# Performance work log

Hardware: AMD Instinct MI355X
Metric: run time of the kernel (lower is better)

Reference implementation:

```python
import jax, jax.numpy as jnp
import numpy as np

N_HEAD = 16
N_STATE = 1024
D_HEAD = N_STATE // N_HEAD
B, T = 4, 2048


def setup_inputs() -> dict:
    key = jax.random.key(0)
    ks = jax.random.split(key, 9)
    x = jax.random.normal(ks[0], (B, T, N_STATE), dtype=jnp.float32)
    # causal additive mask, (T, T)
    neg = jnp.float32(-1e9)
    mask = jnp.where(jnp.tril(jnp.ones((T, T), dtype=bool)), 0.0, neg).astype(jnp.float32)
    s = 0.02  # keep activations in a sane range (module uses torch.randn init)
    Wq = jax.random.normal(ks[1], (N_STATE, N_STATE), dtype=jnp.float32) * s
    bq = jax.random.normal(ks[2], (N_STATE,), dtype=jnp.float32) * s
    Wk = jax.random.normal(ks[3], (N_STATE, N_STATE), dtype=jnp.float32) * s
    Wv = jax.random.normal(ks[4], (N_STATE, N_STATE), dtype=jnp.float32) * s
    bv = jax.random.normal(ks[5], (N_STATE,), dtype=jnp.float32) * s
    Wo = jax.random.normal(ks[6], (N_STATE, N_STATE), dtype=jnp.float32) * s
    bo = jax.random.normal(ks[7], (N_STATE,), dtype=jnp.float32) * s
    return {"x": x, "mask": mask, "Wq": Wq, "bq": bq, "Wk": Wk,
            "Wv": Wv, "bv": bv, "Wo": Wo, "bo": bo}


def reference(x, mask, Wq, bq, Wk, Wv, bv, Wo, bo):
    n, t, _ = x.shape
    scale = D_HEAD ** -0.25
    # projections: Linear stores weight as (out, in), applies x @ W.T
    q = x @ Wq.T + bq
    k = x @ Wk.T          # key has no bias
    v = x @ Wv.T + bv
    # (N, H, T, d)
    q = q.reshape(n, t, N_HEAD, D_HEAD).transpose(0, 2, 1, 3) * scale
    k = k.reshape(n, t, N_HEAD, D_HEAD).transpose(0, 2, 1, 3) * scale
    v = v.reshape(n, t, N_HEAD, D_HEAD).transpose(0, 2, 1, 3)
    qk = jnp.einsum('bhqd,bhkd->bhqk', q, k)
    qk = qk + mask[:t, :t]
    attn = jax.nn.softmax(qk, axis=-1)
    qkv = jnp.einsum('bhqk,bhkd->bhqd', attn, v)
    qkv = qkv.transpose(0, 2, 1, 3).reshape(n, t, N_STATE)
    return qkv @ Wo.T + bo
```

## Files before the change

### kernel.cpp

```cpp
#include <hip/hip_runtime.h>
#include <stdint.h>

#define DEVI __device__ __forceinline__

typedef float        f32x4   __attribute__((ext_vector_type(4)));
typedef float        f32x16  __attribute__((ext_vector_type(16)));
typedef __bf16       bf16x8  __attribute__((ext_vector_type(8)));
typedef unsigned short u16x8 __attribute__((ext_vector_type(8)));
typedef uint32_t     u32x2   __attribute__((ext_vector_type(2)));
typedef uint32_t     u32x4   __attribute__((ext_vector_type(4)));

static constexpr int TSEQ   = 2048;
static constexpr int NSTATE = 1024;
static constexpr int NHEAD  = 16;
static constexpr int DHEAD  = 64;
static constexpr int BATCH  = 4;
static constexpr int MROWS  = BATCH * TSEQ;
static constexpr float QSCALE = 0.125f * 1.44269504088896340736f;
static constexpr float DEFER_THR = 8.0f * 1.44269504088896340736f;

DEVI unsigned short f2bf(float f) {
  union { float f; uint32_t u; } v; v.f = f;
  return (unsigned short)((v.u + 0x7fffu + ((v.u >> 16) & 1u)) >> 16);
}

DEVI uint32_t cvt_pk_bf16(float lo, float hi) {
  uint32_t r;
  asm("v_cvt_pk_bf16_f32 %0, %1, %2" : "=v"(r) : "v"(lo), "v"(hi));
  return r;
}

DEVI f32x4 mfma16(u16x8 a, u16x8 b, f32x4 c) {
  return __builtin_amdgcn_mfma_f32_16x16x32_bf16(
      __builtin_bit_cast(bf16x8, a), __builtin_bit_cast(bf16x8, b), c, 0, 0, 0);
}
DEVI f32x16 mfma32(u16x8 a, u16x8 b, f32x16 c) {
  return __builtin_amdgcn_mfma_f32_32x32x16_bf16(
      __builtin_bit_cast(bf16x8, a), __builtin_bit_cast(bf16x8, b), c, 0, 0, 0);
}

__global__ void cvt_kernel(const float* __restrict__ in,
                           unsigned short* __restrict__ out, int n4) {
  int i = blockIdx.x * blockDim.x + threadIdx.x;
  const int stride = gridDim.x * blockDim.x;
  for (; i < n4; i += stride) {
    const float4 f = ((const float4*)in)[i];
    ushort4 o;
    o.x = f2bf(f.x); o.y = f2bf(f.y); o.z = f2bf(f.z); o.w = f2bf(f.w);
    ((ushort4*)out)[i] = o;
  }
}

__global__ void cvt4_kernel(const float* __restrict__ w0, const float* __restrict__ w1,
                            const float* __restrict__ w2, const float* __restrict__ w3,
                            unsigned short* __restrict__ o0, unsigned short* __restrict__ o1,
                            unsigned short* __restrict__ o2, unsigned short* __restrict__ o3) {
  const int per = NSTATE * NSTATE / 4;
  int i = blockIdx.x * blockDim.x + threadIdx.x;
  const int stride = gridDim.x * blockDim.x;
  for (; i < 4 * per; i += stride) {
    const int wi = i / per, j = i - wi * per;
    const float* src = (wi == 0) ? w0 : (wi == 1) ? w1 : (wi == 2) ? w2 : w3;
    unsigned short* dst = (wi == 0) ? o0 : (wi == 1) ? o1 : (wi == 2) ? o2 : o3;
    const float4 f = ((const float4*)src)[j];
    ushort4 o;
    o.x = f2bf(f.x); o.y = f2bf(f.y); o.z = f2bf(f.z); o.w = f2bf(f.w);
    ((ushort4*)dst)[j] = o;
  }
}

__global__ __launch_bounds__(512)
void gemm_qkv256(const unsigned short* __restrict__ A,
                 const unsigned short* __restrict__ Wqkv,
                 const float* __restrict__ bq, const float* __restrict__ bv,
                 unsigned short* __restrict__ Oqkv)
{
  __shared__ __align__(16) unsigned short As[2][256 * 64];
  __shared__ __align__(16) unsigned short Bs[2][256 * 64];
  const int t = threadIdx.x;
  const int lane = t & 63, wid = t >> 6;
  const int fr = lane & 15, fq = lane >> 4;
  const int wi  = blockIdx.x >> 2;
  const int n0w = (blockIdx.x & 3) * 256;
  const int m0  = blockIdx.y * 256;
  const int wm = wid >> 2, wn = wid & 3;
  const unsigned short* Bw = Wqkv + ((size_t)wi << 20);
  unsigned short* Cq = Oqkv + ((size_t)wi << 23);

  f32x4 acc[8][4] = {};

  const int srow = t >> 3, sg = t & 7;
  const unsigned short* ag = A  + (size_t)(m0  + srow) * NSTATE + sg * 8;
  const unsigned short* bg = Bw + (size_t)(n0w + srow) * NSTATE + sg * 8;
  int wof[4];
  #pragma unroll
  for (int s = 0; s < 4; ++s) {
    const int r = srow + s * 64;
    wof[s] = r * 64 + ((sg ^ (r & 7)) * 8);
  }

  u16x8 sa[4], sb[4];
  #pragma unroll
  for (int s = 0; s < 4; ++s) {
    sa[s] = *(const u16x8*)(ag + (size_t)s * 64 * NSTATE);
    sb[s] = *(const u16x8*)(bg + (size_t)s * 64 * NSTATE);
  }
  #pragma unroll
  for (int s = 0; s < 4; ++s) {
    *(u16x8*)(&As[0][wof[s]]) = sa[s];
    *(u16x8*)(&Bs[0][wof[s]]) = sb[s];
  }

  for (int kt = 0; kt < NSTATE / 64; ++kt) {
    const int cur = kt & 1;
    __syncthreads();
    const bool pre = (kt + 1) < NSTATE / 64;
    if (pre) {
      const int ko = (kt + 1) * 64;
      #pragma unroll
      for (int s = 0; s < 4; ++s) {
        sa[s] = *(const u16x8*)(ag + ko + (size_t)s * 64 * NSTATE);
        sb[s] = *(const u16x8*)(bg + ko + (size_t)s * 64 * NSTATE);
      }
    }
    #pragma unroll
    for (int kk = 0; kk < 2; ++kk) {
      u16x8 af[8], bf[4];
      #pragma unroll
      for (int i = 0; i < 8; ++i) {
        const int r = wm * 128 + i * 16 + fr;
        const int g = (kk * 4 + fq) ^ (r & 7);
        af[i] = *(const u16x8*)(&As[cur][r * 64 + g * 8]);
      }
      #pragma unroll
      for (int j = 0; j < 4; ++j) {
        const int r = wn * 64 + j * 16 + fr;
        const int g = (kk * 4 + fq) ^ (r & 7);
        bf[j] = *(const u16x8*)(&Bs[cur][r * 64 + g * 8]);
      }
      __builtin_amdgcn_s_setprio(1);
      #pragma unroll
      for (int i = 0; i < 8; ++i)
        #pragma unroll
        for (int j = 0; j < 4; ++j)
          acc[i][j] = mfma16(af[i], bf[j], acc[i][j]);
      __builtin_amdgcn_s_setprio(0);
    }
    if (pre) {
      #pragma unroll
      for (int s = 0; s < 4; ++s) {
        *(u16x8*)(&As[cur ^ 1][wof[s]]) = sa[s];
        *(u16x8*)(&Bs[cur ^ 1][wof[s]]) = sb[s];
      }
    }
  }

  const int h = (n0w + wn * 64) >> 6;
  #pragma unroll
  for (int j = 0; j < 4; ++j) {
    const int d = j * 16 + fr;
    const int ncol = n0w + wn * 64 + d;
    const float bj = (wi == 1) ? 0.0f : ((wi == 0) ? bq[ncol] : bv[ncol]);
    #pragma unroll
    for (int i = 0; i < 8; ++i) {
      #pragma unroll
      for (int r = 0; r < 4; ++r) {
        const int row = m0 + wm * 128 + i * 16 + fq * 4 + r;
        const int bb = row >> 11, tt = row & (TSEQ - 1);
        float v = acc[i][j][r] + bj;
        if (wi == 0) v *= QSCALE;
        Cq[(((size_t)(bb * NHEAD + h)) * TSEQ + tt) * DHEAD + d] = f2bf(v);
      }
    }
  }
}

__global__ __launch_bounds__(512)
void gemm_out256(const unsigned short* __restrict__ A,
                 const unsigned short* __restrict__ Bw,
                 const float* __restrict__ bias,
                 float* __restrict__ Co)
{
  __shared__ __align__(16) unsigned short As[2][128 * 64];
  __shared__ __align__(16) unsigned short Bs[2][256 * 64];
  const int t = threadIdx.x;
  const int lane = t & 63, wid = t >> 6;
  const int fr = lane & 15, fq = lane >> 4;
  const int n0 = blockIdx.x * 256;
  const int m0 = blockIdx.y * 128;
  const int wm = wid >> 2, wn = wid & 3;

  f32x4 acc[4][4] = {};

  const int srow = t >> 3, sg = t & 7;
  const unsigned short* ag = A  + (size_t)(m0 + srow) * NSTATE + sg * 8;
  const unsigned short* bg = Bw + (size_t)(n0 + srow) * NSTATE + sg * 8;
  int wof[4];
  #pragma unroll
  for (int s = 0; s < 4; ++s) {
    const int r = srow + s * 64;
    wof[s] = r * 64 + ((sg ^ (r & 7)) * 8);
  }

  u16x8 sa[2], sb[4];
  #pragma unroll
  for (int s = 0; s < 2; ++s)
    sa[s] = *(const u16x8*)(ag + (size_t)s * 64 * NSTATE);
  #pragma unroll
  for (int s = 0; s < 4; ++s)
    sb[s] = *(const u16x8*)(bg + (size_t)s * 64 * NSTATE);
  #pragma unroll
  for (int s = 0; s < 2; ++s) *(u16x8*)(&As[0][wof[s]]) = sa[s];
  #pragma unroll
  for (int s = 0; s < 4; ++s) *(u16x8*)(&Bs[0][wof[s]]) = sb[s];

  for (int kt = 0; kt < NSTATE / 64; ++kt) {
    const int cur = kt & 1;
    __syncthreads();
    const bool pre = (kt + 1) < NSTATE / 64;
    if (pre) {
      const int ko = (kt + 1) * 64;
      #pragma unroll
      for (int s = 0; s < 2; ++s)
        sa[s] = *(const u16x8*)(ag + ko + (size_t)s * 64 * NSTATE);
      #pragma unroll
      for (int s = 0; s < 4; ++s)
        sb[s] = *(const u16x8*)(bg + ko + (size_t)s * 64 * NSTATE);
    }
    #pragma unroll
    for (int kk = 0; kk < 2; ++kk) {
      u16x8 af[4], bf[4];
      #pragma unroll
      for (int i = 0; i < 4; ++i) {
        const int r = wm * 64 + i * 16 + fr;
        const int g = (kk * 4 + fq) ^ (r & 7);
        af[i] = *(const u16x8*)(&As[cur][r * 64 + g * 8]);
      }
      #pragma unroll
      for (int j = 0; j < 4; ++j) {
        const int r = wn * 64 + j * 16 + fr;
        const int g = (kk * 4 + fq) ^ (r & 7);
        bf[j] = *(const u16x8*)(&Bs[cur][r * 64 + g * 8]);
      }
      __builtin_amdgcn_s_setprio(1);
      #pragma unroll
      for (int i = 0; i < 4; ++i)
        #pragma unroll
        for (int j = 0; j < 4; ++j)
          acc[i][j] = mfma16(af[i], bf[j], acc[i][j]);
      __builtin_amdgcn_s_setprio(0);
    }
    if (pre) {
      #pragma unroll
      for (int s = 0; s < 2; ++s) *(u16x8*)(&As[cur ^ 1][wof[s]]) = sa[s];
      #pragma unroll
      for (int s = 0; s < 4; ++s) *(u16x8*)(&Bs[cur ^ 1][wof[s]]) = sb[s];
    }
  }

  #pragma unroll
  for (int j = 0; j < 4; ++j) {
    const int col = n0 + wn * 64 + j * 16 + fr;
    const float bj = bias[col];
    #pragma unroll
    for (int i = 0; i < 4; ++i) {
      const int row0 = m0 + wm * 64 + i * 16 + fq * 4;
      #pragma unroll
      for (int r = 0; r < 4; ++r)
        Co[(size_t)(row0 + r) * NSTATE + col] = acc[i][j][r] + bj;
    }
  }
}

__global__ __launch_bounds__(256)
void flash_attn(const unsigned short* __restrict__ Qg,
                const unsigned short* __restrict__ Kg,
                const unsigned short* __restrict__ Vg,
                unsigned short* __restrict__ O)
{
  const int bh = blockIdx.x;
  const int b  = bh >> 4, h = bh & 15;
  const int t  = threadIdx.x, lane = t & 63, w = t >> 6;
  const int lq = lane & 31, hi = lane >> 5;
  const size_t hoff = (size_t)bh * TSEQ * DHEAD;
  const unsigned short* Qp = Qg + hoff;
  const unsigned short* Kp = Kg + hoff;
  const unsigned short* Vp = Vg + hoff;

  __shared__ __align__(16) unsigned short Kb[2][64 * 64];
  __shared__ __align__(16) unsigned short Vb[2][64 * 64];

  const int skr = t >> 2, skg = t & 3;
  const int svk2 = (t & 31) * 2;
  const int svd  = (t >> 5) * 8;

  #define STAGE_V(buf, va, vb)                                              \
    do {                                                                    \
      const u32x4 vau = __builtin_bit_cast(u32x4, va);                      \
      const u32x4 vbu = __builtin_bit_cast(u32x4, vb);                      \
      _Pragma("unroll")                                                     \
      for (int j = 0; j < 4; ++j) {                                         \
        const uint32_t pe = __builtin_amdgcn_perm(vbu[j], vau[j], 0x05040100); \
        const uint32_t po = __builtin_amdgcn_perm(vbu[j], vau[j], 0x07060302); \
        *(uint32_t*)(&Vb[buf][(svd + 2 * j) * 64 + (svk2 ^ ((2 * j) << 3))]) = pe; \
        *(uint32_t*)(&Vb[buf][(svd + 2 * j + 1) * 64 + (svk2 ^ ((2 * j + 1) << 3))]) = po; \
      }                                                                     \
    } while (0)

  for (int pass = 0; pass < 2; ++pass) {
    const int qb = pass ? (int)blockIdx.y : 15 - (int)blockIdx.y;
    const int qw   = qb * 128 + w * 32;
    const int qrow = qw + lq;

    u16x8 qf[4];
    #pragma unroll
    for (int c = 0; c < 4; ++c)
      qf[c] = *(const u16x8*)(Qp + (size_t)qrow * DHEAD + c * 16 + hi * 8);

    f32x16 oacc[2] = {};
    float m_r = -1e30f, l_r = 0.0f;

    const int nt = (qb + 1) * 2;

    {
      const u16x8 kr0 = *(const u16x8*)(Kp + (size_t)skr * DHEAD + skg * 16);
      const u16x8 kr1 = *(const u16x8*)(Kp + (size_t)skr * DHEAD + skg * 16 + 8);
      const u16x8 va  = *(const u16x8*)(Vp + (size_t)svk2 * DHEAD + svd);
      const u16x8 vb  = *(const u16x8*)(Vp + (size_t)(svk2 + 1) * DHEAD + svd);
      *(u16x8*)(&Kb[0][skr * 64 + (((skg * 2)     ^ (skr & 7)) << 3)]) = kr0;
      *(u16x8*)(&Kb[0][skr * 64 + (((skg * 2 + 1) ^ (skr & 7)) << 3)]) = kr1;
      STAGE_V(0, va, vb);
    }
    __syncthreads();

    for (int kt = 0; kt < nt; ++kt) {
      const int k0 = kt * 64, cur = kt & 1;
      const bool pre = (kt + 1 < nt);
      u16x8 krn0, krn1, van, vbn;
      if (pre) {
        const int k0n = k0 + 64;
        krn0 = *(const u16x8*)(Kp + (size_t)(k0n + skr) * DHEAD + skg * 16);
        krn1 = *(const u16x8*)(Kp + (size_t)(k0n + skr) * DHEAD + skg * 16 + 8);
        van  = *(const u16x8*)(Vp + (size_t)(k0n + svk2) * DHEAD + svd);
        vbn  = *(const u16x8*)(Vp + (size_t)(k0n + svk2 + 1) * DHEAD + svd);
      }

      if (k0 < qw + 32) {
        f32x16 s[2];
        __builtin_amdgcn_s_setprio(1);
        #pragma unroll
        for (int t32 = 0; t32 < 2; ++t32) {
          if (k0 + t32 * 32 < qw + 32) {
            f32x16 z = {};
            #pragma unroll
            for (int c = 0; c < 4; ++c) {
              const u16x8 kf = *(const u16x8*)(
                  &Kb[cur][(t32 * 32 + lq) * 64 + (((2 * c + hi) ^ (lane & 7)) << 3)]);
              z = mfma32(kf, qf[c], z);
            }
            s[t32] = z;
          } else {
            #pragma unroll
            for (int r = 0; r < 16; ++r) s[t32][r] = -1e30f;
          }
        }
        __builtin_amdgcn_s_setprio(0);
        if (k0 + 63 > qw) {
          #pragma unroll
          for (int t32 = 0; t32 < 2; ++t32)
            #pragma unroll
            for (int r = 0; r < 16; ++r) {
              const int kk = k0 + t32 * 32 + (r & 3) + 8 * (r >> 2) + 4 * hi;
              if (kk > qrow) s[t32][r] = -1e30f;
            }
        }

        float mx = fmaxf(s[0][14], s[0][15]);
        #pragma unroll
        for (int r = 0; r < 14; r += 2) mx = fmaxf(fmaxf(mx, s[0][r]), s[0][r + 1]);
        #pragma unroll
        for (int r = 0; r < 16; r += 2) mx = fmaxf(fmaxf(mx, s[1][r]), s[1][r + 1]);
        mx = fmaxf(mx, __shfl_xor(mx, 32));

        if (__any(mx > m_r + DEFER_THR)) {
          const float mnew = fmaxf(m_r, mx);
          const float corr = exp2f(m_r - mnew);
          #pragma unroll
          for (int ds = 0; ds < 2; ++ds)
            #pragma unroll
            for (int r = 0; r < 16; ++r) oacc[ds][r] *= corr;
          l_r *= corr;
          m_r = mnew;
        }

        float ps = 0.0f;
        uint32_t pk[2][8];
        #pragma unroll
        for (int t32 = 0; t32 < 2; ++t32)
          #pragma unroll
          for (int m2 = 0; m2 < 8; ++m2) {
            const float pa = exp2f(s[t32][2 * m2]     - m_r);
            const float pb = exp2f(s[t32][2 * m2 + 1] - m_r);
            ps += pa + pb;
            pk[t32][m2] = cvt_pk_bf16(pa, pb);
          }
        ps += __shfl_xor(ps, 32);
        l_r += ps;

        uint32_t pf[2][2][4];
        #pragma unroll
        for (int t32 = 0; t32 < 2; ++t32)
          #pragma unroll
          for (int hf = 0; hf < 2; ++hf) {
            const u32x2 r02 = __builtin_amdgcn_permlane32_swap(
                pk[t32][hf * 4 + 0], pk[t32][hf * 4 + 2], false, false);
            const u32x2 r13 = __builtin_amdgcn_permlane32_swap(
                pk[t32][hf * 4 + 1], pk[t32][hf * 4 + 3], false, false);
            pf[t32][hf][0] = r02.x; pf[t32][hf][2] = r02.y;
            pf[t32][hf][1] = r13.x; pf[t32][hf][3] = r13.y;
          }

        __builtin_amdgcn_s_setprio(1);
        #pragma unroll
        for (int c = 0; c < 4; ++c) {
          if (k0 + 16 * c < qw + 32) {
            const u32x4 pw = {pf[c >> 1][c & 1][0], pf[c >> 1][c & 1][1],
                              pf[c >> 1][c & 1][2], pf[c >> 1][c & 1][3]};
            const u16x8 pv = __builtin_bit_cast(u16x8, pw);
            #pragma unroll
            for (int ds = 0; ds < 2; ++ds) {
              const u16x8 vf = *(const u16x8*)(
                  &Vb[cur][(ds * 32 + lq) * 64 + (((2 * c + hi) ^ (lq & 7)) << 3)]);
              oacc[ds] = mfma32(vf, pv, oacc[ds]);
            }
          }
        }
        __builtin_amdgcn_s_setprio(0);
      }

      if (pre) {
        *(u16x8*)(&Kb[cur ^ 1][skr * 64 + (((skg * 2)     ^ (skr & 7)) << 3)]) = krn0;
        *(u16x8*)(&Kb[cur ^ 1][skr * 64 + (((skg * 2 + 1) ^ (skr & 7)) << 3)]) = krn1;
        STAGE_V(cur ^ 1, van, vbn);
      }
      __syncthreads();
    }

    const float inv = 1.0f / l_r;
    const size_t base = ((size_t)(b * TSEQ + qrow)) * NSTATE + h * DHEAD;
    #pragma unroll
    for (int ds = 0; ds < 2; ++ds)
      #pragma unroll
      for (int m2 = 0; m2 < 8; ++m2) {
        const int d = ds * 32 + 2 * (m2 & 1) + 8 * (m2 >> 1) + 4 * hi;
        *(uint32_t*)(O + base + d) =
            cvt_pk_bf16(oacc[ds][2 * m2] * inv, oacc[ds][2 * m2 + 1] * inv);
      }
  }
  #undef STAGE_V
}

extern "C" void kernel_launch(void* const* d_in, const int* in_sizes, int n_in,
                              void* d_out, int out_size, void* d_ws, size_t ws_size,
                              hipStream_t stream)
{
  (void)in_sizes; (void)n_in; (void)out_size; (void)ws_size;
  const float* x  = (const float*)d_in[0];
  const float* Wq = (const float*)d_in[2];
  const float* bq = (const float*)d_in[3];
  const float* Wk = (const float*)d_in[4];
  const float* Wv = (const float*)d_in[5];
  const float* bv = (const float*)d_in[6];
  const float* Wo = (const float*)d_in[7];
  const float* bo = (const float*)d_in[8];

  char* ws = (char*)d_ws;
  unsigned short* xb  = (unsigned short*)(ws);
  unsigned short* wqb = (unsigned short*)(ws + (16u << 20));
  unsigned short* wkb = wqb + (1u << 20);
  unsigned short* wvb = wkb + (1u << 20);
  unsigned short* wob = wvb + (1u << 20);
  unsigned short* qb_ = (unsigned short*)(ws + (24u << 20));
  unsigned short* kb_ = (unsigned short*)(ws + (40u << 20));
  unsigned short* vb_ = (unsigned short*)(ws + (56u << 20));

  cvt_kernel<<<2048, 256, 0, stream>>>(x,  xb,  MROWS * NSTATE / 4);
  cvt4_kernel<<<2048, 256, 0, stream>>>(Wq, Wk, Wv, Wo, wqb, wkb, wvb, wob);

  gemm_qkv256<<<dim3(12, MROWS / 256), 512, 0, stream>>>(xb, wqb, bq, bv, qb_);

  flash_attn<<<dim3(BATCH * NHEAD, 8), 256, 0, stream>>>(qb_, kb_, vb_, xb);

  gemm_out256<<<dim3(NSTATE / 256, MROWS / 128), 512, 0, stream>>>(xb, wob, bo, (float*)d_out);
}
```

Baseline: 202.6 us.

## Process both causal query blocks in one KV sweep and merge conversion kernels

The flash attention kernel now holds two query blocks (a long one and a short one) in registers at once and sweeps the K/V tiles a single time, applying each block's tile computation while the tiles are resident. Before, the two blocks ran in two separate passes that each reloaded K/V. This removes the duplicated K/V loads and staging, at the cost of doubling the accumulator and Q-fragment register footprint, which may lower occupancy. It also merges the x and weight bf16 conversion kernels into one launch and swaps exp2f for a raw v_exp_f32 instruction. An unused global-to-LDS load helper is added.

```diff
diff --git a/kernel.cpp b/kernel.cpp
--- a/kernel.cpp
+++ b/kernel.cpp
@@ -29,6 +29,11 @@
   asm("v_cvt_pk_bf16_f32 %0, %1, %2" : "=v"(r) : "v"(lo), "v"(hi));
   return r;
 }
+DEVI float fexp2(float x) {
+  float r;
+  asm("v_exp_f32 %0, %1" : "=v"(r) : "v"(x));
+  return r;
+}
 
 DEVI f32x4 mfma16(u16x8 a, u16x8 b, f32x4 c) {
   return __builtin_amdgcn_mfma_f32_16x16x32_bf16(
@@ -39,29 +44,34 @@
       __builtin_bit_cast(bf16x8, a), __builtin_bit_cast(bf16x8, b), c, 0, 0, 0);
 }
 
-__global__ void cvt_kernel(const float* __restrict__ in,
-                           unsigned short* __restrict__ out, int n4) {
+DEVI void gload_lds16(const void* g, void* l) {
+  __builtin_amdgcn_global_load_lds(
+      (const __attribute__((address_space(1))) void*)g,
+      (__attribute__((address_space(3))) void*)l, 16, 0, 0);
+}
+
+__global__ void cvt_all(const float* __restrict__ x,
+                        const float* __restrict__ w0, const float* __restrict__ w1,
+                        const float* __restrict__ w2, const float* __restrict__ w3,
+                        unsigned short* __restrict__ xb,
+                        unsigned short* __restrict__ wb)
+{
+  const int NX = (MROWS * NSTATE) / 4;
+  const int NW = (NSTATE * NSTATE) / 4;
+  const int total = NX + 4 * NW;
   int i = blockIdx.x * blockDim.x + threadIdx.x;
   const int stride = gridDim.x * blockDim.x;
-  for (; i < n4; i += stride) {
-    const float4 f = ((const float4*)in)[i];
-    ushort4 o;
-    o.x = f2bf(f.x); o.y = f2bf(f.y); o.z = f2bf(f.z); o.w = f2bf(f.w);
-    ((ushort4*)out)[i] = o;
-  }
-}
-
-__global__ void cvt4_kernel(const float* __restrict__ w0, const float* __restrict__ w1,
-                            const float* __restrict__ w2, const float* __restrict__ w3,
-                            unsigned short* __restrict__ o0, unsigned short* __restrict__ o1,
-                            unsigned short* __restrict__ o2, unsigned short* __restrict__ o3) {
-  const int per = NSTATE * NSTATE / 4;
-  int i = blockIdx.x * blockDim.x + threadIdx.x;
-  const int stride = gridDim.x * blockDim.x;
-  for (; i < 4 * per; i += stride) {
-    const int wi = i / per, j = i - wi * per;
-    const float* src = (wi == 0) ? w0 : (wi == 1) ? w1 : (wi == 2) ? w2 : w3;
-    unsigned short* dst = (wi == 0) ? o0 : (wi == 1) ? o1 : (wi == 2) ? o2 : o3;
+  for (; i < total; i += stride) {
+    const float* src;
+    unsigned short* dst;
+    int j;
+    if (i < NX) { src = x; dst = xb; j = i; }
+    else {
+      const int k = i - NX, wi = k >> 18;
+      src = (wi == 0) ? w0 : (wi == 1) ? w1 : (wi == 2) ? w2 : w3;
+      dst = wb + ((size_t)wi << 20);
+      j = k & (NW - 1);
+    }
     const float4 f = ((const float4*)src)[j];
     ushort4 o;
     o.x = f2bf(f.x); o.y = f2bf(f.y); o.z = f2bf(f.z); o.w = f2bf(f.w);
@@ -279,6 +289,8 @@
                 unsigned short* __restrict__ O)
 {
   const int bh = blockIdx.x;
+  const int y  = blockIdx.y;
+  const int qbA = 15 - y, qbB = y;
   const int b  = bh >> 4, h = bh & 15;
   const int t  = threadIdx.x, lane = t & 63, w = t >> 6;
   const int lq = lane & 31, hi = lane >> 5;
@@ -289,6 +301,19 @@
 
   __shared__ __align__(16) unsigned short Kb[2][64 * 64];
   __shared__ __align__(16) unsigned short Vb[2][64 * 64];
+
+  const int qwA = qbA * 128 + w * 32, qrowA = qwA + lq;
+  const int qwB = qbB * 128 + w * 32, qrowB = qwB + lq;
+
+  u16x8 qfA[4], qfB[4];
+  #pragma unroll
+  for (int c = 0; c < 4; ++c) {
+    qfA[c] = *(const u16x8*)(Qp + (size_t)qrowA * DHEAD + c * 16 + hi * 8);
+    qfB[c] = *(const u16x8*)(Qp + (size_t)qrowB * DHEAD + c * 16 + hi * 8);
+  }
+
+  f32x16 oaccA[2] = {}, oaccB[2] = {};
+  float mA = -1e30f, lA = 0.0f, mB = -1e30f, lB = 0.0f;
 
   const int skr = t >> 2, skg = t & 3;
   const int svk2 = (t & 31) * 2;
@@ -307,156 +332,155 @@
       }                                                                     \
     } while (0)
 
-  for (int pass = 0; pass < 2; ++pass) {
-    const int qb = pass ? (int)blockIdx.y : 15 - (int)blockIdx.y;
-    const int qw   = qb * 128 + w * 32;
-    const int qrow = qw + lq;
-
-    u16x8 qf[4];
-    #pragma unroll
-    for (int c = 0; c < 4; ++c)
-      qf[c] = *(const u16x8*)(Qp + (size_t)qrow * DHEAD + c * 16 + hi * 8);
-
-    f32x16 oacc[2] = {};
-    float m_r = -1e30f, l_r = 0.0f;
-
-    const int nt = (qb + 1) * 2;
-
-    {
-      const u16x8 kr0 = *(const u16x8*)(Kp + (size_t)skr * DHEAD + skg * 16);
-      const u16x8 kr1 = *(const u16x8*)(Kp + (size_t)skr * DHEAD + skg * 16 + 8);
-      const u16x8 va  = *(const u16x8*)(Vp + (size_t)svk2 * DHEAD + svd);
-      const u16x8 vb  = *(const u16x8*)(Vp + (size_t)(svk2 + 1) * DHEAD + svd);
-      *(u16x8*)(&Kb[0][skr * 64 + (((skg * 2)     ^ (skr & 7)) << 3)]) = kr0;
-      *(u16x8*)(&Kb[0][skr * 64 + (((skg * 2 + 1) ^ (skr & 7)) << 3)]) = kr1;
-      STAGE_V(0, va, vb);
+  #define ATTN_TILE(qw_, qrow_, qf_, oacc_, m_, l_)                          \
+    do {                                                                     \
+      f32x16 s[2];                                                           \
+      __builtin_amdgcn_s_setprio(1);                                         \
+      _Pragma("unroll")                                                      \
+      for (int t32 = 0; t32 < 2; ++t32) {                                    \
+        if (k0 + t32 * 32 < (qw_) + 32) {                                    \
+          f32x16 z = {};                                                     \
+          _Pragma("unroll")                                                  \
+          for (int c = 0; c < 4; ++c) {                                      \
+            const u16x8 kf = *(const u16x8*)(                                \
+                &Kb[cur][(t32 * 32 + lq) * 64 + (((2 * c + hi) ^ (lane & 7)) << 3)]); \
+            z = mfma32(kf, (qf_)[c], z);                                     \
+          }                                                                  \
+          s[t32] = z;                                                        \
+        } else {                                                             \
+          _Pragma("unroll")                                                  \
+          for (int r = 0; r < 16; ++r) s[t32][r] = -1e30f;                   \
+        }                                                                    \
+      }                                                                      \
+      __builtin_amdgcn_s_setprio(0);                                         \
+      if (k0 + 63 > (qw_)) {                                                 \
+        _Pragma("unroll")                                                    \
+        for (int t32 = 0; t32 < 2; ++t32)                                    \
+          _Pragma("unroll")                                                  \
+          for (int r = 0; r < 16; ++r) {                                     \
+            const int kk = k0 + t32 * 32 + (r & 3) + 8 * (r >> 2) + 4 * hi;  \
+            if (kk > (qrow_)) s[t32][r] = -1e30f;                            \
+          }                                                                  \
+      }                                                                      \
+      float mx = fmaxf(s[0][14], s[0][15]);                                  \
+      _Pragma("unroll")                                                      \
+      for (int r = 0; r < 14; r += 2) mx = fmaxf(fmaxf(mx, s[0][r]), s[0][r + 1]); \
+      _Pragma("unroll")                                                      \
+      for (int r = 0; r < 16; r += 2) mx = fmaxf(fmaxf(mx, s[1][r]), s[1][r + 1]); \
+      mx = fmaxf(mx, __shfl_xor(mx, 32));                                    \
+      if (__any(mx > (m_) + DEFER_THR)) {                                    \
+        const float mnew = fmaxf((m_), mx);                                  \
+        const float corr = fexp2((m_) - mnew);                               \
+        _Pragma("unroll")                                                    \
+        for (int ds = 0; ds < 2; ++ds)                                       \
+          _Pragma("unroll")                                                  \
+          for (int r = 0; r < 16; ++r) (oacc_)[ds][r] *= corr;               \
+        (l_) *= corr;                                                        \
+        (m_) = mnew;                                                         \
+      }                                                                      \
+      float ps = 0.0f;                                                       \
+      uint32_t pk[2][8];                                                     \
+      _Pragma("unroll")                                                      \
+      for (int t32 = 0; t32 < 2; ++t32)                                      \
+        _Pragma("unroll")                                                    \
+        for (int m2 = 0; m2 < 8; ++m2) {                                     \
+          const float pa = fexp2(s[t32][2 * m2]     - (m_));                 \
+          const float pb = fexp2(s[t32][2 * m2 + 1] - (m_));                 \
+          ps += pa + pb;                                                     \
+          pk[t32][m2] = cvt_pk_bf16(pa, pb);                                 \
+        }                                                                    \
+      ps += __shfl_xor(ps, 32);                                              \
+      (l_) += ps;                                                            \
+      uint32_t pf[2][2][4];                                                  \
+      _Pragma("unroll")                                                      \
+      for (int t32 = 0; t32 < 2; ++t32)                                      \
+        _Pragma("unroll")                                                    \
+        for (int hf = 0; hf < 2; ++hf) {                                     \
+          const u32x2 r02 = __builtin_amdgcn_permlane32_swap(                \
+              pk[t32][hf * 4 + 0], pk[t32][hf * 4 + 2], false, false);       \
+          const u32x2 r13 = __builtin_amdgcn_permlane32_swap(                \
+              pk[t32][hf * 4 + 1], pk[t32][hf * 4 + 3], false, false);       \
+          pf[t32][hf][0] = r02.x; pf[t32][hf][2] = r02.y;                    \
+          pf[t32][hf][1] = r13.x; pf[t32][hf][3] = r13.y;                    \
+        }                                                                    \
+      __builtin_amdgcn_s_setprio(1);                                         \
+      _Pragma("unroll")                                                      \
+      for (int c = 0; c < 4; ++c) {                                          \
+        if (k0 + 16 * c < (qw_) + 32) {                                      \
+          const u32x4 pw = {pf[c >> 1][c & 1][0], pf[c >> 1][c & 1][1],      \
+                            pf[c >> 1][c & 1][2], pf[c >> 1][c & 1][3]};     \
+          const u16x8 pv = __builtin_bit_cast(u16x8, pw);                    \
+          _Pragma("unroll")                                                  \
+          for (int ds = 0; ds < 2; ++ds) {                                   \
+            const u16x8 vf = *(const u16x8*)(                                \
+                &Vb[cur][(ds * 32 + lq) * 64 + (((2 * c + hi) ^ (lq & 7)) << 3)]); \
+            (oacc_)[ds] = mfma32(vf, pv, (oacc_)[ds]);                       \
+          }                                                                  \
+        }                                                                    \
+      }                                                                      \
+      __builtin_amdgcn_s_setprio(0);                                         \
+    } while (0)
+
+  {
+    const u16x8 kr0 = *(const u16x8*)(Kp + (size_t)skr * DHEAD + skg * 16);
+    const u16x8 kr1 = *(const u16x8*)(Kp + (size_t)skr * DHEAD + skg * 16 + 8);
+    const u16x8 va  = *(const u16x8*)(Vp + (size_t)svk2 * DHEAD + svd);
+    const u16x8 vb  = *(const u16x8*)(Vp + (size_t)(svk2 + 1) * DHEAD + svd);
+    *(u16x8*)(&Kb[0][skr * 64 + (((skg * 2)     ^ (skr & 7)) << 3)]) = kr0;
+    *(u16x8*)(&Kb[0][skr * 64 + (((skg * 2 + 1) ^ (skr & 7)) << 3)]) = kr1;
+    STAGE_V(0, va, vb);
+  }
+  __syncthreads();
+
+  const int nt = (qbA + 1) * 2;
+  for (int kt = 0; kt < nt; ++kt) {
+    const int k0 = kt * 64, cur = kt & 1;
+    const bool pre = (kt + 1 < nt);
+    u16x8 krn0, krn1, van, vbn;
+    if (pre) {
+      const int k0n = k0 + 64;
+      krn0 = *(const u16x8*)(Kp + (size_t)(k0n + skr) * DHEAD + skg * 16);
+      krn1 = *(const u16x8*)(Kp + (size_t)(k0n + skr) * DHEAD + skg * 16 + 8);
+      van  = *(const u16x8*)(Vp + (size_t)(k0n + svk2) * DHEAD + svd);
+      vbn  = *(const u16x8*)(Vp + (size_t)(k0n + svk2 + 1) * DHEAD + svd);
+    }
+
+    if (k0 < qwA + 32) ATTN_TILE(qwA, qrowA, qfA, oaccA, mA, lA);
+    if (k0 < qwB + 32) ATTN_TILE(qwB, qrowB, qfB, oaccB, mB, lB);
+
+    if (pre) {
+      *(u16x8*)(&Kb[cur ^ 1][skr * 64 + (((skg * 2)     ^ (skr & 7)) << 3)]) = krn0;
+      *(u16x8*)(&Kb[cur ^ 1][skr * 64 + (((skg * 2 + 1) ^ (skr & 7)) << 3)]) = krn1;
+      STAGE_V(cur ^ 1, van, vbn);
     }
     __syncthreads();
-
-    for (int kt = 0; kt < nt; ++kt) {
-      const int k0 = kt * 64, cur = kt & 1;
-      const bool pre = (kt + 1 < nt);
-      u16x8 krn0, krn1, van, vbn;
-      if (pre) {
-        const int k0n = k0 + 64;
-        krn0 = *(const u16x8*)(Kp + (size_t)(k0n + skr) * DHEAD + skg * 16);
-        krn1 = *(const u16x8*)(Kp + (size_t)(k0n + skr) * DHEAD + skg * 16 + 8);
-        van  = *(const u16x8*)(Vp + (size_t)(k0n + svk2) * DHEAD + svd);
-        vbn  = *(const u16x8*)(Vp + (size_t)(k0n + svk2 + 1) * DHEAD + svd);
-      }
-
-      if (k0 < qw + 32) {
-        f32x16 s[2];
-        __builtin_amdgcn_s_setprio(1);
-        #pragma unroll
-        for (int t32 = 0; t32 < 2; ++t32) {
-          if (k0 + t32 * 32 < qw + 32) {
-            f32x16 z = {};
-            #pragma unroll
-            for (int c = 0; c < 4; ++c) {
-              const u16x8 kf = *(const u16x8*)(
-                  &Kb[cur][(t32 * 32 + lq) * 64 + (((2 * c + hi) ^ (lane & 7)) << 3)]);
-              z = mfma32(kf, qf[c], z);
-            }
-            s[t32] = z;
-          } else {
-            #pragma unroll
-            for (int r = 0; r < 16; ++r) s[t32][r] = -1e30f;
-          }
-        }
-        __builtin_amdgcn_s_setprio(0);
-        if (k0 + 63 > qw) {
-          #pragma unroll
-          for (int t32 = 0; t32 < 2; ++t32)
-            #pragma unroll
-            for (int r = 0; r < 16; ++r) {
-              const int kk = k0 + t32 * 32 + (r & 3) + 8 * (r >> 2) + 4 * hi;
-              if (kk > qrow) s[t32][r] = -1e30f;
-            }
-        }
-
-        float mx = fmaxf(s[0][14], s[0][15]);
-        #pragma unroll
-        for (int r = 0; r < 14; r += 2) mx = fmaxf(fmaxf(mx, s[0][r]), s[0][r + 1]);
-        #pragma unroll
-        for (int r = 0; r < 16; r += 2) mx = fmaxf(fmaxf(mx, s[1][r]), s[1][r + 1]);
-        mx = fmaxf(mx, __shfl_xor(mx, 32));
-
-        if (__any(mx > m_r + DEFER_THR)) {
-          const float mnew = fmaxf(m_r, mx);
-          const float corr = exp2f(m_r - mnew);
-          #pragma unroll
-          for (int ds = 0; ds < 2; ++ds)
-            #pragma unroll
-            for (int r = 0; r < 16; ++r) oacc[ds][r] *= corr;
-          l_r *= corr;
-          m_r = mnew;
-        }
-
-        float ps = 0.0f;
-        uint32_t pk[2][8];
-        #pragma unroll
-        for (int t32 = 0; t32 < 2; ++t32)
-          #pragma unroll
-          for (int m2 = 0; m2 < 8; ++m2) {
-            const float pa = exp2f(s[t32][2 * m2]     - m_r);
-            const float pb = exp2f(s[t32][2 * m2 + 1] - m_r);
-            ps += pa + pb;
-            pk[t32][m2] = cvt_pk_bf16(pa, pb);
-          }
-        ps += __shfl_xor(ps, 32);
-        l_r += ps;
-
-        uint32_t pf[2][2][4];
-        #pragma unroll
-        for (int t32 = 0; t32 < 2; ++t32)
-          #pragma unroll
-          for (int hf = 0; hf < 2; ++hf) {
-            const u32x2 r02 = __builtin_amdgcn_permlane32_swap(
-                pk[t32][hf * 4 + 0], pk[t32][hf * 4 + 2], false, false);
-            const u32x2 r13 = __builtin_amdgcn_permlane32_swap(
-                pk[t32][hf * 4 + 1], pk[t32][hf * 4 + 3], false, false);
-            pf[t32][hf][0] = r02.x; pf[t32][hf][2] = r02.y;
-            pf[t32][hf][1] = r13.x; pf[t32][hf][3] = r13.y;
-          }
-
-        __builtin_amdgcn_s_setprio(1);
-        #pragma unroll
-        for (int c = 0; c < 4; ++c) {
-          if (k0 + 16 * c < qw + 32) {
-            const u32x4 pw = {pf[c >> 1][c & 1][0], pf[c >> 1][c & 1][1],
-                              pf[c >> 1][c & 1][2], pf[c >> 1][c & 1][3]};
-            const u16x8 pv = __builtin_bit_cast(u16x8, pw);
-            #pragma unroll
-            for (int ds = 0; ds < 2; ++ds) {
-              const u16x8 vf = *(const u16x8*)(
-                  &Vb[cur][(ds * 32 + lq) * 64 + (((2 * c + hi) ^ (lq & 7)) << 3)]);
-              oacc[ds] = mfma32(vf, pv, oacc[ds]);
-            }
-          }
-        }
-        __builtin_amdgcn_s_setprio(0);
-      }
-
-      if (pre) {
-        *(u16x8*)(&Kb[cur ^ 1][skr * 64 + (((skg * 2)     ^ (skr & 7)) << 3)]) = krn0;
-        *(u16x8*)(&Kb[cur ^ 1][skr * 64 + (((skg * 2 + 1) ^ (skr & 7)) << 3)]) = krn1;
-        STAGE_V(cur ^ 1, van, vbn);
-      }
-      __syncthreads();
-    }
-
-    const float inv = 1.0f / l_r;
-    const size_t base = ((size_t)(b * TSEQ + qrow)) * NSTATE + h * DHEAD;
+  }
+
+  {
+    const float inv = 1.0f / lA;
+    const size_t base = ((size_t)(b * TSEQ + qrowA)) * NSTATE + h * DHEAD;
     #pragma unroll
     for (int ds = 0; ds < 2; ++ds)
       #pragma unroll
       for (int m2 = 0; m2 < 8; ++m2) {
         const int d = ds * 32 + 2 * (m2 & 1) + 8 * (m2 >> 1) + 4 * hi;
         *(uint32_t*)(O + base + d) =
-            cvt_pk_bf16(oacc[ds][2 * m2] * inv, oacc[ds][2 * m2 + 1] * inv);
-      }
-  }
+            cvt_pk_bf16(oaccA[ds][2 * m2] * inv, oaccA[ds][2 * m2 + 1] * inv);
+      }
+  }
+  {
+    const float inv = 1.0f / lB;
+    const size_t base = ((size_t)(b * TSEQ + qrowB)) * NSTATE + h * DHEAD;
+    #pragma unroll
+    for (int ds = 0; ds < 2; ++ds)
+      #pragma unroll
+      for (int m2 = 0; m2 < 8; ++m2) {
+        const int d = ds * 32 + 2 * (m2 & 1) + 8 * (m2 >> 1) + 4 * hi;
+        *(uint32_t*)(O + base + d) =
+            cvt_pk_bf16(oaccB[ds][2 * m2] * inv, oaccB[ds][2 * m2 + 1] * inv);
+      }
+  }
+  #undef ATTN_TILE
   #undef STAGE_V
 }
 
@@ -477,15 +501,12 @@
   char* ws = (char*)d_ws;
   unsigned short* xb  = (unsigned short*)(ws);
   unsigned short* wqb = (unsigned short*)(ws + (16u << 20));
-  unsigned short* wkb = wqb + (1u << 20);
-  unsigned short* wvb = wkb + (1u << 20);
-  unsigned short* wob = wvb + (1u << 20);
+  unsigned short* wob = wqb + (3u << 20);
   unsigned short* qb_ = (unsigned short*)(ws + (24u << 20));
   unsigned short* kb_ = (unsigned short*)(ws + (40u << 20));
   unsigned short* vb_ = (unsigned short*)(ws + (56u << 20));
 
-  cvt_kernel<<<2048, 256, 0, stream>>>(x,  xb,  MROWS * NSTATE / 4);
-  cvt4_kernel<<<2048, 256, 0, stream>>>(Wq, Wk, Wv, Wo, wqb, wkb, wvb, wob);
+  cvt_all<<<2048, 256, 0, stream>>>(x, Wq, Wk, Wv, Wo, xb, wqb);
 
   gemm_qkv256<<<dim3(12, MROWS / 256), 512, 0, stream>>>(xb, wqb, bq, bv, qb_);
 
```

After: 228.2 us. 12.6% more time.
